# Optimization experiments

Measured on AMD Instinct MI355X. Metric: run time of the kernel, lower is better.

The kernel has to match this reference:

```python
import jax, jax.numpy as jnp
import numpy as np

N_GROUP = 1024
K_GROUP = 64
RADIUS = 0.2
BN_EPS = 1e-5
D_FEATURES = [6, 64, 64, 128]


def _fps(coord, n_group):
    # Farthest point sampling. coord: [B, N, 3] -> indices [B, n_group]
    B, N, _ = coord.shape

    def step(carry, _):
        dist, far = carry
        centroid = jax.vmap(lambda c, i: c[i])(coord, far)  # [B, 3]
        d = jnp.sum((coord - centroid[:, None, :]) ** 2, axis=-1)  # [B, N]
        dist = jnp.minimum(dist, d)
        nfar = jnp.argmax(dist, axis=-1).astype(jnp.int32)
        return (dist, nfar), far

    init = (jnp.full((B, N), 1e10, coord.dtype), jnp.zeros((B,), jnp.int32))
    _, idxs = jax.lax.scan(step, init, None, length=n_group)
    return idxs.T  # [B, n_group]


def _ball_query(coord, new_xyz, k, radius):
    # coord: [B, N, 3], new_xyz: [B, S, 3] -> idx [B, S, k]
    N = coord.shape[1]
    sqr = jnp.sum((new_xyz[:, :, None, :] - coord[:, None, :, :]) ** 2, axis=-1)  # [B,S,N]
    idx = jnp.where(sqr > radius * radius, N, jnp.arange(N, dtype=jnp.int32))
    idx = jnp.sort(idx, axis=-1)[:, :, :k]
    first = idx[:, :, :1]
    return jnp.where(idx == N, first, idx)  # pad empty slots with first in-ball index


def _gather(x, idx):
    # x: [B, N, C], idx: [B, ...] -> [B, ..., C]
    return jax.vmap(lambda a, i: a[i])(x, idx)


def _conv_bn_relu(x, W, b, g, beta):
    # 1x1 Conv2d: x [B, Cin, S, K], W [Cout, Cin]
    y = jnp.einsum('oc,bcsk->bosk', W, x) + b[None, :, None, None]
    mean = jnp.mean(y, axis=(0, 2, 3), keepdims=True)
    var = jnp.var(y, axis=(0, 2, 3), keepdims=True)  # biased, matches torch BN train
    y = (y - mean) * jax.lax.rsqrt(var + BN_EPS)
    return jax.nn.relu(y * g[None, :, None, None] + beta[None, :, None, None])


def setup_inputs() -> dict:
    key = jax.random.key(0)
    ks = jax.random.split(key, 16)
    B, N = 16, 4096
    inp = {
        'feature': jax.random.normal(ks[0], (B, 3, N), jnp.float32),
        'coord': jax.random.uniform(ks[1], (B, 3, N), jnp.float32),
    }
    for li, (cin, cout) in enumerate(zip(D_FEATURES[:-1], D_FEATURES[1:])):
        scale = 1.0 / np.sqrt(cin)
        inp[f'W{li}'] = jax.random.uniform(ks[2 + 4 * li], (cout, cin), jnp.float32, -scale, scale)
        inp[f'b{li}'] = jax.random.uniform(ks[3 + 4 * li], (cout,), jnp.float32, -scale, scale)
        inp[f'g{li}'] = jnp.ones((cout,), jnp.float32)
        inp[f'beta{li}'] = jnp.zeros((cout,), jnp.float32)
    return inp


def reference(feature, coord, W0, b0, g0, beta0, W1, b1, g1, beta1, W2, b2, g2, beta2):
    # feature: [B, d_in, N], coord: [B, 3, N]
    feat = jnp.transpose(feature, (0, 2, 1))  # [B, N, d_in]
    xyz = jnp.transpose(coord, (0, 2, 1))     # [B, N, 3]

    fps_idx = _fps(xyz, N_GROUP)                      # [B, S]
    new_xyz = _gather(xyz, fps_idx)                   # [B, S, 3]
    nbr_idx = _ball_query(xyz, new_xyz, K_GROUP, RADIUS)  # [B, S, K]

    grouped_xyz = _gather(xyz, nbr_idx) - new_xyz[:, :, None, :]  # [B, S, K, 3]
    grouped_feat = _gather(feat, nbr_idx)                          # [B, S, K, d_in]
    grouped = jnp.concatenate([grouped_xyz, grouped_feat], axis=-1)  # [B, S, K, 6]

    x = jnp.transpose(grouped, (0, 3, 1, 2))  # [B, C, S, K]
    x = _conv_bn_relu(x, W0, b0, g0, beta0)
    x = _conv_bn_relu(x, W1, b1, g1, beta1)
    x = _conv_bn_relu(x, W2, b2, g2, beta2)
    out_feat = jnp.max(x, axis=-1)  # [B, d_out, S]
    out_coord = jnp.transpose(new_xyz, (0, 2, 1))  # [B, 3, S]
    return (out_feat, out_coord)
```

## Files before the change

kernel.cpp:

```cpp
#include <hip/hip_runtime.h>
#include <hip/hip_bf16.h>
#include <math.h>

#define NB 16
#define NPT 4096
#define NS 1024
#define NK 64
#define CNTF 1048576.0f
#define R2C 0.04f
#define BNEPS 1e-5f

#define OFF_NEWXYZ 0
#define OFF_X1     49152
#define OFF_STATS  6340608
#define NCOPY 32
#define ST_LEN 8352
#define OFF_FOLD   6607872
#define ST_M1 0
#define ST_G1 6
#define ST_M2 27
#define ST_G2 91
#define ST_M3 4187
#define ST_G3 4251
#define F_W0 0
#define F_B0 384
#define F_W1 448
#define F_B1 4544
#define F_W2 4608
#define F_B2 12800
#define OUTC_OFF 2097152

typedef __attribute__((ext_vector_type(8))) short s8v;
typedef __attribute__((ext_vector_type(4))) short s4v;
typedef __attribute__((ext_vector_type(4))) float f4v;

__device__ __forceinline__ float bf2f(short s) {
  return __uint_as_float(((unsigned)(unsigned short)s) << 16);
}
__device__ __forceinline__ short f2bf(float f) {
  unsigned u = __float_as_uint(f);
  return (short)((u + 0x7fff + ((u >> 16) & 1)) >> 16);
}
__device__ __forceinline__ int SW(int p) {
  return (((p) & 7) << 1) | (((p) >> 3) & 1);
}
__device__ __forceinline__ f4v mm(s8v a, s8v b, f4v c) {
  return __builtin_amdgcn_mfma_f32_16x16x32_bf16(a, b, c, 0, 0, 0);
}
__device__ __forceinline__ s8v ldB_pc(const short* x, int t, int l, int kb) {
  int p = t * 16 + (l & 15);
  int c0 = kb + 4 * (l >> 4);
  int base = p << 6;
  s4v a = *(const s4v*)&x[base + ((((c0) >> 2) ^ SW(p)) << 2)];
  s4v b = *(const s4v*)&x[base + ((((c0 + 16) >> 2) ^ SW(p)) << 2)];
  s8v r; r[0]=a[0]; r[1]=a[1]; r[2]=a[2]; r[3]=a[3]; r[4]=b[0]; r[5]=b[1]; r[6]=b[2]; r[7]=b[3];
  return r;
}
__device__ __forceinline__ s8v ldG_cp(const short* x, int ct, int l, int pb) {
  int c = ct * 16 + (l & 15);
  int p0 = pb + 4 * (l >> 4);
  int base = c << 6;
  s4v a = *(const s4v*)&x[base + ((((p0) >> 2) ^ SW(c)) << 2)];
  s4v b = *(const s4v*)&x[base + ((((p0 + 16) >> 2) ^ SW(c)) << 2)];
  s8v r; r[0]=a[0]; r[1]=a[1]; r[2]=a[2]; r[3]=a[3]; r[4]=b[0]; r[5]=b[1]; r[6]=b[2]; r[7]=b[3];
  return r;
}
__device__ __forceinline__ s8v mkWfrag(const float* W, int row, int kb, int l) {
  int c0 = kb + 4 * (l >> 4);
  s8v f;
#pragma unroll
  for (int j = 0; j < 4; ++j) f[j] = f2bf(W[row * 64 + c0 + j]);
#pragma unroll
  for (int j = 0; j < 4; ++j) f[4 + j] = f2bf(W[row * 64 + c0 + 16 + j]);
  return f;
}
__device__ __forceinline__ s8v onesfrag() {
  s8v f;
#pragma unroll
  for (int j = 0; j < 8; ++j) f[j] = (short)0x3F80;
  return f;
}
__device__ __forceinline__ float rowmax16(float x) {
#define DPPMAX(ctrl)                                                          \
  x = fmaxf(x, __int_as_float(__builtin_amdgcn_update_dpp(                    \
             0, __float_as_int(x), ctrl, 0xf, 0xf, true)))
  DPPMAX(0x111); DPPMAX(0x112); DPPMAX(0x114); DPPMAX(0x118);
#undef DPPMAX
  return x;
}

__launch_bounds__(512)
__global__ void k_fps(const float* __restrict__ coord, float* __restrict__ newxyz,
                      float* __restrict__ out_coord) {
#pragma clang fp contract(off)
  __shared__ float4 sxyz[NPT];
  __shared__ int sel[NS];
  __shared__ unsigned long long skey[2][8];
  int b = blockIdx.x;
  int tid = threadIdx.x;
  int w = tid >> 6, lane = tid & 63;
  const float* cb = coord + (size_t)b * 3 * NPT;
  for (int i = tid; i < NPT; i += 512)
    sxyz[i] = make_float4(cb[i], cb[NPT + i], cb[2 * NPT + i], 0.f);
  __syncthreads();
  float px[8], py[8], pz[8], dd[8];
  int base = tid * 8;
#pragma unroll
  for (int j = 0; j < 8; ++j) {
    float4 p = sxyz[base + j];
    px[j] = p.x; py[j] = p.y; pz[j] = p.z; dd[j] = 1e10f;
  }
  if (tid == 0) sel[0] = 0;
  float4 c0 = sxyz[0];
  float cx = c0.x, cy = c0.y, cz = c0.z;
  for (int it = 1; it < NS; ++it) {
    float nd[8];
#pragma unroll
    for (int j = 0; j < 8; ++j) {
      float dx = px[j] - cx, dy = py[j] - cy, dz = pz[j] - cz;
      float d = dx * dx; d = d + dy * dy; d = d + dz * dz;
      float v = fminf(dd[j], d); dd[j] = v; nd[j] = v;
    }
    float bv = nd[0];
#pragma unroll
    for (int j = 1; j < 8; ++j) bv = fmaxf(bv, nd[j]);
    int bj = 7;
#pragma unroll
    for (int j = 6; j >= 0; --j) bj = (nd[j] == bv) ? j : bj;
    int bi = base + bj;
    float rm = rowmax16(bv);
    float r0 = __int_as_float(__builtin_amdgcn_readlane(__float_as_int(rm), 15));
    float r1 = __int_as_float(__builtin_amdgcn_readlane(__float_as_int(rm), 31));
    float r2 = __int_as_float(__builtin_amdgcn_readlane(__float_as_int(rm), 47));
    float r3 = __int_as_float(__builtin_amdgcn_readlane(__float_as_int(rm), 63));
    float wmax = fmaxf(fmaxf(r0, r1), fmaxf(r2, r3));
    unsigned long long mm2 = __ballot(bv == wmax);
    int lead = (int)__builtin_ctzll(mm2);
    int wbi = __builtin_amdgcn_readlane(bi, lead);
    int par = it & 1;
    if (lane == 0)
      skey[par][w] = ((unsigned long long)__float_as_uint(wmax) << 32) |
                     (unsigned)(4095 - wbi);
    __syncthreads();
    unsigned long long g = skey[par][0];
#pragma unroll
    for (int q = 1; q < 8; ++q) {
      unsigned long long o = skey[par][q];
      g = g > o ? g : o;
    }
    int fi = 4095 - (int)(g & 0xffffffffu);
    if (tid == 0) sel[it] = fi;
    float4 cc = sxyz[fi];
    cx = cc.x; cy = cc.y; cz = cc.z;
  }
  __syncthreads();
  for (int s = tid; s < NS; s += 512) {
    int i = sel[s];
    float4 p = sxyz[i];
    newxyz[((size_t)b * NS + s) * 3 + 0] = p.x;
    newxyz[((size_t)b * NS + s) * 3 + 1] = p.y;
    newxyz[((size_t)b * NS + s) * 3 + 2] = p.z;
    out_coord[((size_t)b * 3 + 0) * NS + s] = p.x;
    out_coord[((size_t)b * 3 + 1) * NS + s] = p.y;
    out_coord[((size_t)b * 3 + 2) * NS + s] = p.z;
  }
}

__launch_bounds__(256)
__global__ void k_group(const float* __restrict__ coord, const float* __restrict__ feat,
                        const float* __restrict__ newxyz, float* __restrict__ x1) {
#pragma clang fp contract(off)
  __shared__ float st[4][6][64];
  int tid = threadIdx.x;
  int w = tid >> 6, lane = tid & 63;
  int g = blockIdx.x * 4 + w;
  int b = g >> 10;
  const float* cb = coord + (size_t)b * 3 * NPT;
  const float* fb = feat + (size_t)b * 3 * NPT;
  float cx = newxyz[(size_t)g * 3 + 0], cy = newxyz[(size_t)g * 3 + 1], cz = newxyz[(size_t)g * 3 + 2];
  int cnt = 0;
  float x = cb[lane], y = cb[NPT + lane], z = cb[2 * NPT + lane];
  for (int ch = 0; ch < NPT / 64 && cnt < 64; ++ch) {
    float xn = 0.f, yn = 0.f, zn = 0.f;
    if (ch + 1 < NPT / 64) {
      int pn = (ch + 1) * 64 + lane;
      xn = cb[pn]; yn = cb[NPT + pn]; zn = cb[2 * NPT + pn];
    }
    int p = ch * 64 + lane;
    float dx = x - cx, dy = y - cy, dz = z - cz;
    float d = dx * dx; d = d + dy * dy; d = d + dz * dz;
    bool in = (d <= R2C);
    unsigned long long m = __ballot(in);
    int rank = __popcll(m & ((1ull << lane) - 1ull));
    int slot = cnt + rank;
    if (in && slot < 64) {
      st[w][0][slot] = dx; st[w][1][slot] = dy; st[w][2][slot] = dz;
      st[w][3][slot] = fb[p]; st[w][4][slot] = fb[NPT + p]; st[w][5][slot] = fb[2 * NPT + p];
    }
    cnt += (int)__popcll(m);
    x = xn; y = yn; z = zn;
  }
  __syncthreads();
  cnt = min(cnt, 64);
  if (lane >= cnt) {
#pragma unroll
    for (int c = 0; c < 6; ++c) st[w][c][lane] = st[w][c][0];
  }
  float* dst = x1 + (size_t)g * 384;
#pragma unroll
  for (int c = 0; c < 6; ++c) dst[c * 64 + lane] = st[w][c][lane];
}

__launch_bounds__(256)
__global__ void k_stats1(const float* __restrict__ x1, float* __restrict__ stats) {
  float* st = stats + (size_t)(blockIdx.x & (NCOPY - 1)) * ST_LEN;
  float m[6] = {0, 0, 0, 0, 0, 0};
  float gacc[21];
#pragma unroll
  for (int q = 0; q < 21; ++q) gacc[q] = 0.f;
  int nth = gridDim.x * 256;
  for (int col = blockIdx.x * 256 + threadIdx.x; col < NB * NS * NK; col += nth) {
    int g = col >> 6, k = col & 63;
    const float* p = x1 + (size_t)g * 384;
    float v[6];
#pragma unroll
    for (int c = 0; c < 6; ++c) v[c] = p[c * 64 + k];
    int q = 0;
#pragma unroll
    for (int c = 0; c < 6; ++c) {
      m[c] += v[c];
#pragma unroll
      for (int c2 = c; c2 < 6; ++c2) { gacc[q] += v[c] * v[c2]; q++; }
    }
  }
#pragma unroll
  for (int c = 0; c < 6; ++c) {
    float t = m[c];
    for (int o = 1; o < 64; o <<= 1) t += __shfl_xor(t, o);
    if ((threadIdx.x & 63) == 0) atomicAdd(&st[ST_M1 + c], t);
  }
#pragma unroll
  for (int q = 0; q < 21; ++q) {
    float t = gacc[q];
    for (int o = 1; o < 64; o <<= 1) t += __shfl_xor(t, o);
    if ((threadIdx.x & 63) == 0) atomicAdd(&st[ST_G1 + q], t);
  }
}

__launch_bounds__(256)
__global__ void k_fold1(const float* __restrict__ W0, const float* __restrict__ b0,
                        const float* __restrict__ g0, const float* __restrict__ be0,
                        const float* __restrict__ stats, float* __restrict__ fold) {
  __shared__ float sMG[27];
  int tid = threadIdx.x;
  if (tid < 27) {
    float s = 0.f;
    for (int cp = 0; cp < NCOPY; ++cp) s += stats[(size_t)cp * ST_LEN + tid];
    sMG[tid] = s;
  }
  __syncthreads();
  int o = tid;
  if (o >= 64) return;
  float G[6][6], mu[6];
  {
    int q = 0;
    for (int c = 0; c < 6; ++c)
      for (int c2 = c; c2 < 6; ++c2) { float v = sMG[ST_G1 + q] / CNTF; G[c][c2] = v; G[c2][c] = v; q++; }
    for (int c = 0; c < 6; ++c) mu[c] = sMG[ST_M1 + c] / CNTF;
  }
  float w[6];
  for (int c = 0; c < 6; ++c) w[c] = W0[o * 6 + c];
  float bb = b0[o];
  float s1 = 0.f, ey2 = 0.f;
  for (int c = 0; c < 6; ++c) {
    s1 += w[c] * mu[c];
    for (int c2 = 0; c2 < 6; ++c2) ey2 += w[c] * w[c2] * G[c][c2];
  }
  float muy = s1 + bb;
  ey2 = ey2 + 2.f * bb * s1 + bb * bb;
  float var = ey2 - muy * muy;
  float sc = g0[o] / sqrtf(var + BNEPS);
  for (int c = 0; c < 6; ++c) fold[F_W0 + o * 6 + c] = w[c] * sc;
  fold[F_B0 + o] = (bb - muy) * sc + be0[o];
}

__launch_bounds__(256)
__global__ void k_fold2(const float* __restrict__ W1, const float* __restrict__ b1,
                        const float* __restrict__ g1, const float* __restrict__ be1,
                        const float* __restrict__ stats, float* __restrict__ fold) {
  __shared__ float sG[4096];
  __shared__ float sM[64];
  int tid = threadIdx.x;
  for (int i = tid; i < 4096; i += 256) {
    float s = 0.f;
    for (int cp = 0; cp < NCOPY; ++cp) s += stats[(size_t)cp * ST_LEN + ST_G2 + i];
    sG[i] = s;
  }
  if (tid < 64) {
    float s = 0.f;
    for (int cp = 0; cp < NCOPY; ++cp) s += stats[(size_t)cp * ST_LEN + ST_M2 + tid];
    sM[tid] = s;
  }
  __syncthreads();
  int o = tid;
  if (o >= 64) return;
  float s1 = 0.f, ey2 = 0.f;
  for (int c = 0; c < 64; ++c) {
    float w = W1[o * 64 + c];
    s1 += w * sM[c];
    float t = 0.f;
    for (int c2 = 0; c2 < 64; ++c2) t += W1[o * 64 + c2] * sG[c * 64 + c2];
    ey2 += w * t;
  }
  s1 /= CNTF; ey2 /= CNTF;
  float bb = b1[o];
  float muy = s1 + bb;
  ey2 = ey2 + 2.f * bb * s1 + bb * bb;
  float var = ey2 - muy * muy;
  float sc = g1[o] / sqrtf(var + BNEPS);
  for (int c = 0; c < 64; ++c) fold[F_W1 + o * 64 + c] = W1[o * 64 + c] * sc;
  fold[F_B1 + o] = (bb - muy) * sc + be1[o];
}

__launch_bounds__(256)
__global__ void k_fold3(const float* __restrict__ W2, const float* __restrict__ b2,
                        const float* __restrict__ g2, const float* __restrict__ be2,
                        const float* __restrict__ stats, float* __restrict__ fold) {
  __shared__ float sG[4096];
  __shared__ float sM[64];
  int tid = threadIdx.x;
  for (int i = tid; i < 4096; i += 256) {
    float s = 0.f;
    for (int cp = 0; cp < NCOPY; ++cp) s += stats[(size_t)cp * ST_LEN + ST_G3 + i];
    sG[i] = s;
  }
  if (tid < 64) {
    float s = 0.f;
    for (int cp = 0; cp < NCOPY; ++cp) s += stats[(size_t)cp * ST_LEN + ST_M3 + tid];
    sM[tid] = s;
  }
  __syncthreads();
  int o = tid;
  if (o >= 128) return;
  float s1 = 0.f, ey2 = 0.f;
  for (int c = 0; c < 64; ++c) {
    float w = W2[o * 64 + c];
    s1 += w * sM[c];
    float t = 0.f;
    for (int c2 = 0; c2 < 64; ++c2) t += W2[o * 64 + c2] * sG[c * 64 + c2];
    ey2 += w * t;
  }
  s1 /= CNTF; ey2 /= CNTF;
  float bb = b2[o];
  float muy = s1 + bb;
  ey2 = ey2 + 2.f * bb * s1 + bb * bb;
  float var = ey2 - muy * muy;
  float sc = g2[o] / sqrtf(var + BNEPS);
  for (int c = 0; c < 64; ++c) fold[F_W2 + o * 64 + c] = W2[o * 64 + c] * sc;
  fold[F_B2 + o] = (bb - muy) * sc + be2[o];
}

__device__ __forceinline__ void x2_to_pc(const float* x1s, const float* wf0, const float* bf0,
                                         short* x2p, int tid) {
  int p = tid & 63, r = tid >> 6;
  float xin[6];
#pragma unroll
  for (int c = 0; c < 6; ++c) xin[c] = x1s[c * 64 + p];
#pragma unroll
  for (int m4 = 0; m4 < 4; ++m4) {
    s4v v;
#pragma unroll
    for (int u = 0; u < 4; ++u) {
      int o = r * 16 + m4 * 4 + u;
      float a = bf0[o];
#pragma unroll
      for (int c = 0; c < 6; ++c) a += wf0[o * 6 + c] * xin[c];
      v[u] = f2bf(fmaxf(a, 0.f));
    }
    int cb = r * 16 + m4 * 4;
    *(s4v*)&x2p[(p << 6) + (((cb >> 2) ^ SW(p)) << 2)] = v;
  }
}
__device__ __forceinline__ void x2_to_cp(const float* x1s, const float* wf0, const float* bf0,
                                         short* x2c, int tid) {
  int p = tid & 63, r = tid >> 6;
  float xin[6];
#pragma unroll
  for (int c = 0; c < 6; ++c) xin[c] = x1s[c * 64 + p];
#pragma unroll
  for (int i = 0; i < 16; ++i) {
    int o = r * 16 + i;
    float a = bf0[o];
#pragma unroll
    for (int c = 0; c < 6; ++c) a += wf0[o * 6 + c] * xin[c];
    x2c[(o << 6) + (((p >> 2) ^ SW(o)) << 2) + (p & 3)] = f2bf(fmaxf(a, 0.f));
  }
}

__launch_bounds__(256)
__global__ void k_pass2(const float* __restrict__ x1, const float* __restrict__ fold,
                        float* __restrict__ stats) {
  __shared__ float x1s[384];
  __shared__ float wf0s[384];
  __shared__ float bf0s[64];
  __shared__ short x2c[4096];
  int tid = threadIdx.x;
  int lane = tid & 63, w = tid >> 6;
  float* st = stats + (size_t)(blockIdx.x & (NCOPY - 1)) * ST_LEN;
  for (int i = tid; i < 384; i += 256) wf0s[i] = fold[F_W0 + i];
  if (tid < 64) bf0s[tid] = fold[F_B0 + tid];
  s8v ones = onesfrag();
  f4v gacc[4] = {};
  f4v maccv = {};
  for (int rep = 0; rep < 32; ++rep) {
    int g = blockIdx.x + rep * 512;
    __syncthreads();
    for (int i = tid; i < 384; i += 256) x1s[i] = x1[(size_t)g * 384 + i];
    __syncthreads();
    x2_to_cp(x1s, wf0s, bf0s, x2c, tid);
    __syncthreads();
#pragma unroll
    for (int pb = 0; pb < 64; pb += 32) {
      s8v a = ldG_cp(x2c, w, lane, pb);
      maccv = mm(a, ones, maccv);
#pragma unroll
      for (int ct = 0; ct < 4; ++ct)
        gacc[ct] = mm(a, ldG_cp(x2c, ct, lane, pb), gacc[ct]);
    }
  }
#pragma unroll
  for (int ct = 0; ct < 4; ++ct)
#pragma unroll
    for (int r = 0; r < 4; ++r) {
      int row = 16 * w + 4 * (lane >> 4) + r;
      int col = 16 * ct + (lane & 15);
      atomicAdd(&st[ST_G2 + row * 64 + col], gacc[ct][r]);
    }
  if ((lane & 15) == 0)
#pragma unroll
    for (int r = 0; r < 4; ++r)
      atomicAdd(&st[ST_M2 + 16 * w + 4 * (lane >> 4) + r], maccv[r]);
}

__launch_bounds__(256)
__global__ void k_pass3(const float* __restrict__ x1, const float* __restrict__ fold,
                        float* __restrict__ stats) {
  __shared__ float x1s[384];
  __shared__ float wf0s[384];
  __shared__ float bf0s[64];
  __shared__ short x2p[4096];
  __shared__ short x3c[4096];
  int tid = threadIdx.x;
  int lane = tid & 63, w = tid >> 6;
  float* st = stats + (size_t)(blockIdx.x & (NCOPY - 1)) * ST_LEN;
  for (int i = tid; i < 384; i += 256) wf0s[i] = fold[F_W0 + i];
  if (tid < 64) bf0s[tid] = fold[F_B0 + tid];
  s8v w1f[2];
  float bias2[4];
#pragma unroll
  for (int s = 0; s < 2; ++s) w1f[s] = mkWfrag(fold + F_W1, 16 * w + (lane & 15), 32 * s, lane);
#pragma unroll
  for (int r = 0; r < 4; ++r) bias2[r] = fold[F_B1 + 16 * w + 4 * (lane >> 4) + r];
  s8v ones = onesfrag();
  f4v gacc[4] = {};
  f4v maccv = {};
  for (int rep = 0; rep < 32; ++rep) {
    int g = blockIdx.x + rep * 512;
    __syncthreads();
    for (int i = tid; i < 384; i += 256) x1s[i] = x1[(size_t)g * 384 + i];
    __syncthreads();
    x2_to_pc(x1s, wf0s, bf0s, x2p, tid);
    __syncthreads();
#pragma unroll
    for (int t = 0; t < 4; ++t) {
      f4v acc; acc[0] = bias2[0]; acc[1] = bias2[1]; acc[2] = bias2[2]; acc[3] = bias2[3];
      acc = mm(w1f[0], ldB_pc(x2p, t, lane, 0), acc);
      acc = mm(w1f[1], ldB_pc(x2p, t, lane, 32), acc);
      int p = 16 * t + (lane & 15);
#pragma unroll
      for (int r = 0; r < 4; ++r) {
        int c = 16 * w + 4 * (lane >> 4) + r;
        x3c[(c << 6) + (((p >> 2) ^ SW(c)) << 2) + (p & 3)] = f2bf(fmaxf(acc[r], 0.f));
      }
    }
    __syncthreads();
#pragma unroll
    for (int pb = 0; pb < 64; pb += 32) {
      s8v a = ldG_cp(x3c, w, lane, pb);
      maccv = mm(a, ones, maccv);
#pragma unroll
      for (int ct = 0; ct < 4; ++ct)
        gacc[ct] = mm(a, ldG_cp(x3c, ct, lane, pb), gacc[ct]);
    }
  }
#pragma unroll
  for (int ct = 0; ct < 4; ++ct)
#pragma unroll
    for (int r = 0; r < 4; ++r) {
      int row = 16 * w + 4 * (lane >> 4) + r;
      int col = 16 * ct + (lane & 15);
      atomicAdd(&st[ST_G3 + row * 64 + col], gacc[ct][r]);
    }
  if ((lane & 15) == 0)
#pragma unroll
    for (int r = 0; r < 4; ++r)
      atomicAdd(&st[ST_M3 + 16 * w + 4 * (lane >> 4) + r], maccv[r]);
}

__launch_bounds__(256)
__global__ void k_final(const float* __restrict__ x1, const float* __restrict__ fold,
                        float* __restrict__ out) {
  __shared__ float x1s[384];
  __shared__ float wf0s[384];
  __shared__ float bf0s[64];
  __shared__ short x2p[4096];
  __shared__ short x3p[4096];
  int tid = threadIdx.x;
  int lane = tid & 63, w = tid >> 6;
  for (int i = tid; i < 384; i += 256) wf0s[i] = fold[F_W0 + i];
  if (tid < 64) bf0s[tid] = fold[F_B0 + tid];
  s8v w1f[2], w2f[2][2];
  float bias2[4], bias3[2][4];
#pragma unroll
  for (int s = 0; s < 2; ++s) w1f[s] = mkWfrag(fold + F_W1, 16 * w + (lane & 15), 32 * s, lane);
#pragma unroll
  for (int r = 0; r < 4; ++r) bias2[r] = fold[F_B1 + 16 * w + 4 * (lane >> 4) + r];
#pragma unroll
  for (int ot = 0; ot < 2; ++ot) {
#pragma unroll
    for (int s = 0; s < 2; ++s)
      w2f[ot][s] = mkWfrag(fold + F_W2, 16 * (2 * w + ot) + (lane & 15), 32 * s, lane);
#pragma unroll
    for (int r = 0; r < 4; ++r) bias3[ot][r] = fold[F_B2 + 16 * (2 * w + ot) + 4 * (lane >> 4) + r];
  }
  for (int rep = 0; rep < 8; ++rep) {
    int g = blockIdx.x + rep * 2048;
    int b = g >> 10, s = g & 1023;
    __syncthreads();
    for (int i = tid; i < 384; i += 256) x1s[i] = x1[(size_t)g * 384 + i];
    __syncthreads();
    x2_to_pc(x1s, wf0s, bf0s, x2p, tid);
    __syncthreads();
#pragma unroll
    for (int t = 0; t < 4; ++t) {
      f4v acc; acc[0] = bias2[0]; acc[1] = bias2[1]; acc[2] = bias2[2]; acc[3] = bias2[3];
      acc = mm(w1f[0], ldB_pc(x2p, t, lane, 0), acc);
      acc = mm(w1f[1], ldB_pc(x2p, t, lane, 32), acc);
      s4v v;
#pragma unroll
      for (int r = 0; r < 4; ++r) v[r] = f2bf(fmaxf(acc[r], 0.f));
      int p = 16 * t + (lane & 15);
      int cb = 16 * w + 4 * (lane >> 4);
      *(s4v*)&x3p[(p << 6) + (((cb >> 2) ^ SW(p)) << 2)] = v;
    }
    __syncthreads();
    float vmax[2][4];
#pragma unroll
    for (int t = 0; t < 4; ++t) {
      s8v b0f = ldB_pc(x3p, t, lane, 0);
      s8v b1f = ldB_pc(x3p, t, lane, 32);
#pragma unroll
      for (int ot = 0; ot < 2; ++ot) {
        f4v acc; acc[0] = bias3[ot][0]; acc[1] = bias3[ot][1]; acc[2] = bias3[ot][2]; acc[3] = bias3[ot][3];
        acc = mm(w2f[ot][0], b0f, acc);
        acc = mm(w2f[ot][1], b1f, acc);
#pragma unroll
        for (int r = 0; r < 4; ++r)
          vmax[ot][r] = (t == 0) ? acc[r] : fmaxf(vmax[ot][r], acc[r]);
      }
    }
#pragma unroll
    for (int ot = 0; ot < 2; ++ot)
#pragma unroll
      for (int r = 0; r < 4; ++r) {
        float m = rowmax16(vmax[ot][r]);
        if ((lane & 15) == 15) {
          int o = 16 * (2 * w + ot) + 4 * (lane >> 4) + r;
          out[((size_t)b * 128 + o) * NS + s] = fmaxf(m, 0.f);
        }
      }
  }
}

extern "C" void kernel_launch(void* const* d_in, const int* in_sizes, int n_in,
                              void* d_out, int out_size, void* d_ws, size_t ws_size,
                              hipStream_t stream) {
  (void)in_sizes; (void)n_in; (void)out_size; (void)ws_size;
  const float* feature = (const float*)d_in[0];
  const float* coord = (const float*)d_in[1];
  const float* W0 = (const float*)d_in[2];  const float* b0 = (const float*)d_in[3];
  const float* g0 = (const float*)d_in[4];  const float* be0 = (const float*)d_in[5];
  const float* W1 = (const float*)d_in[6];  const float* b1 = (const float*)d_in[7];
  const float* g1 = (const float*)d_in[8];  const float* be1 = (const float*)d_in[9];
  const float* W2 = (const float*)d_in[10]; const float* b2 = (const float*)d_in[11];
  const float* g2 = (const float*)d_in[12]; const float* be2 = (const float*)d_in[13];
  float* out = (float*)d_out;
  float* ws = (float*)d_ws;
  float* newxyz = ws + OFF_NEWXYZ;
  float* x1 = ws + OFF_X1;
  float* stats = ws + OFF_STATS;
  float* fold = ws + OFF_FOLD;
  hipMemsetAsync(stats, 0, (size_t)NCOPY * ST_LEN * sizeof(float), stream);
  hipLaunchKernelGGL(k_fps, dim3(NB), dim3(512), 0, stream, coord, newxyz, out + OUTC_OFF);
  hipLaunchKernelGGL(k_group, dim3(4096), dim3(256), 0, stream, coord, feature, newxyz, x1);
  hipLaunchKernelGGL(k_stats1, dim3(256), dim3(256), 0, stream, x1, stats);
  hipLaunchKernelGGL(k_fold1, dim3(1), dim3(256), 0, stream, W0, b0, g0, be0, stats, fold);
  hipLaunchKernelGGL(k_pass2, dim3(512), dim3(256), 0, stream, x1, fold, stats);
  hipLaunchKernelGGL(k_fold2, dim3(1), dim3(256), 0, stream, W1, b1, g1, be1, stats, fold);
  hipLaunchKernelGGL(k_pass3, dim3(512), dim3(256), 0, stream, x1, fold, stats);
  hipLaunchKernelGGL(k_fold3, dim3(1), dim3(256), 0, stream, W2, b2, g2, be2, stats, fold);
  hipLaunchKernelGGL(k_final, dim3(2048), dim3(256), 0, stream, x1, fold, out);
}
```

Baseline: 1.079 ms.

## Shrink FPS block to 4 waves and broadcast winning centroid coords directly

```diff
diff --git a/kernel.cpp b/kernel.cpp
--- a/kernel.cpp
+++ b/kernel.cpp
@@ -89,74 +89,83 @@
   return x;
 }
 
-__launch_bounds__(512)
+__launch_bounds__(256)
 __global__ void k_fps(const float* __restrict__ coord, float* __restrict__ newxyz,
                       float* __restrict__ out_coord) {
 #pragma clang fp contract(off)
-  __shared__ float4 sxyz[NPT];
-  __shared__ int sel[NS];
-  __shared__ unsigned long long skey[2][8];
+  __shared__ float4 snew[NS];
+  __shared__ uint4 skeyA[2][4];
+  __shared__ float skeyZ[2][4];
   int b = blockIdx.x;
   int tid = threadIdx.x;
   int w = tid >> 6, lane = tid & 63;
   const float* cb = coord + (size_t)b * 3 * NPT;
-  for (int i = tid; i < NPT; i += 512)
-    sxyz[i] = make_float4(cb[i], cb[NPT + i], cb[2 * NPT + i], 0.f);
-  __syncthreads();
-  float px[8], py[8], pz[8], dd[8];
-  int base = tid * 8;
-#pragma unroll
-  for (int j = 0; j < 8; ++j) {
-    float4 p = sxyz[base + j];
-    px[j] = p.x; py[j] = p.y; pz[j] = p.z; dd[j] = 1e10f;
-  }
-  if (tid == 0) sel[0] = 0;
-  float4 c0 = sxyz[0];
-  float cx = c0.x, cy = c0.y, cz = c0.z;
+  float px[16], py[16], pz[16], dd[16];
+  int base = tid * 16;
+#pragma unroll
+  for (int j = 0; j < 16; ++j) {
+    px[j] = cb[base + j];
+    py[j] = cb[NPT + base + j];
+    pz[j] = cb[2 * NPT + base + j];
+    dd[j] = 1e10f;
+  }
+  float cx = cb[0], cy = cb[NPT], cz = cb[2 * NPT];
+  if (tid == 0) snew[0] = make_float4(cx, cy, cz, 0.f);
   for (int it = 1; it < NS; ++it) {
-    float nd[8];
-#pragma unroll
-    for (int j = 0; j < 8; ++j) {
+    float nd[16];
+#pragma unroll
+    for (int j = 0; j < 16; ++j) {
       float dx = px[j] - cx, dy = py[j] - cy, dz = pz[j] - cz;
       float d = dx * dx; d = d + dy * dy; d = d + dz * dz;
       float v = fminf(dd[j], d); dd[j] = v; nd[j] = v;
     }
     float bv = nd[0];
 #pragma unroll
-    for (int j = 1; j < 8; ++j) bv = fmaxf(bv, nd[j]);
-    int bj = 7;
-#pragma unroll
-    for (int j = 6; j >= 0; --j) bj = (nd[j] == bv) ? j : bj;
-    int bi = base + bj;
+    for (int j = 1; j < 16; ++j) bv = fmaxf(bv, nd[j]);
+    int bj = 15;
+#pragma unroll
+    for (int j = 14; j >= 0; --j) bj = (nd[j] == bv) ? j : bj;
     float rm = rowmax16(bv);
     float r0 = __int_as_float(__builtin_amdgcn_readlane(__float_as_int(rm), 15));
     float r1 = __int_as_float(__builtin_amdgcn_readlane(__float_as_int(rm), 31));
     float r2 = __int_as_float(__builtin_amdgcn_readlane(__float_as_int(rm), 47));
     float r3 = __int_as_float(__builtin_amdgcn_readlane(__float_as_int(rm), 63));
     float wmax = fmaxf(fmaxf(r0, r1), fmaxf(r2, r3));
-    unsigned long long mm2 = __ballot(bv == wmax);
-    int lead = (int)__builtin_ctzll(mm2);
-    int wbi = __builtin_amdgcn_readlane(bi, lead);
+    unsigned long long mmk = __ballot(bv == wmax);
+    int lead = (int)__builtin_ctzll(mmk);
     int par = it & 1;
-    if (lane == 0)
-      skey[par][w] = ((unsigned long long)__float_as_uint(wmax) << 32) |
-                     (unsigned)(4095 - wbi);
-    __syncthreads();
-    unsigned long long g = skey[par][0];
-#pragma unroll
-    for (int q = 1; q < 8; ++q) {
-      unsigned long long o = skey[par][q];
-      g = g > o ? g : o;
-    }
-    int fi = 4095 - (int)(g & 0xffffffffu);
-    if (tid == 0) sel[it] = fi;
-    float4 cc = sxyz[fi];
-    cx = cc.x; cy = cc.y; cz = cc.z;
+    if (lane == lead) {
+      unsigned long long key =
+          ((unsigned long long)__float_as_uint(bv) << 32) |
+          (unsigned)(4095 - (base + bj));
+      skeyA[par][w] = make_uint4((unsigned)key, (unsigned)(key >> 32),
+                                 __float_as_uint(px[bj]), __float_as_uint(py[bj]));
+      skeyZ[par][w] = pz[bj];
+    }
+    __syncthreads();
+    uint4 e0 = skeyA[par][0], e1 = skeyA[par][1], e2 = skeyA[par][2], e3 = skeyA[par][3];
+    float z0 = skeyZ[par][0], z1 = skeyZ[par][1], z2 = skeyZ[par][2], z3 = skeyZ[par][3];
+    unsigned long long k0 = ((unsigned long long)e0.y << 32) | e0.x;
+    unsigned long long k1 = ((unsigned long long)e1.y << 32) | e1.x;
+    unsigned long long k2 = ((unsigned long long)e2.y << 32) | e2.x;
+    unsigned long long k3 = ((unsigned long long)e3.y << 32) | e3.x;
+    bool s01 = k1 > k0;
+    unsigned long long ka = s01 ? k1 : k0;
+    unsigned xa = s01 ? e1.z : e0.z, ya = s01 ? e1.w : e0.w;
+    float za = s01 ? z1 : z0;
+    bool s23 = k3 > k2;
+    unsigned long long kb2 = s23 ? k3 : k2;
+    unsigned xb = s23 ? e3.z : e2.z, yb = s23 ? e3.w : e2.w;
+    float zb = s23 ? z3 : z2;
+    bool sf = kb2 > ka;
+    cx = __uint_as_float(sf ? xb : xa);
+    cy = __uint_as_float(sf ? yb : ya);
+    cz = sf ? zb : za;
+    if (tid == 0) snew[it] = make_float4(cx, cy, cz, 0.f);
   }
   __syncthreads();
-  for (int s = tid; s < NS; s += 512) {
-    int i = sel[s];
-    float4 p = sxyz[i];
+  for (int s = tid; s < NS; s += 256) {
+    float4 p = snew[s];
     newxyz[((size_t)b * NS + s) * 3 + 0] = p.x;
     newxyz[((size_t)b * NS + s) * 3 + 1] = p.y;
     newxyz[((size_t)b * NS + s) * 3 + 2] = p.z;
@@ -601,7 +610,7 @@
   float* stats = ws + OFF_STATS;
   float* fold = ws + OFF_FOLD;
   hipMemsetAsync(stats, 0, (size_t)NCOPY * ST_LEN * sizeof(float), stream);
-  hipLaunchKernelGGL(k_fps, dim3(NB), dim3(512), 0, stream, coord, newxyz, out + OUTC_OFF);
+  hipLaunchKernelGGL(k_fps, dim3(NB), dim3(256), 0, stream, coord, newxyz, out + OUTC_OFF);
   hipLaunchKernelGGL(k_group, dim3(4096), dim3(256), 0, stream, coord, feature, newxyz, x1);
   hipLaunchKernelGGL(k_stats1, dim3(256), dim3(256), 0, stream, x1, stats);
   hipLaunchKernelGGL(k_fold1, dim3(1), dim3(256), 0, stream, W0, b0, g0, be0, stats, fold);
```

New measurement: 1.645 ms. +52.4%, slower.
